# Kernel tuning notes

Hardware: AMD Instinct MI355X
Metric: run time of the kernel (lower is better)

Reference implementation:

```python
import jax, jax.numpy as jnp
import numpy as np

HEADS, OUT = 4, 64  # GATConv(heads=4, out_channels=64, concat=False)
NEG_SLOPE = 0.2


def gat_conv(x, src, dst, num_nodes, W, att_src, att_dst, bias):
    # x: [N, Fin]; W: [Fin, H*C]; att_*: [H, C]; bias: [C]
    N = num_nodes
    H, C = att_src.shape
    h = (x @ W).reshape(N, H, C)                      # per-head projections
    a_s = jnp.einsum('nhc,hc->nh', h, att_src)        # [N, H]
    a_d = jnp.einsum('nhc,hc->nh', h, att_dst)        # [N, H]
    e = jax.nn.leaky_relu(a_s[src] + a_d[dst], NEG_SLOPE)   # [E, H]
    # segment softmax over destination nodes (self-loops guarantee nonempty segments)
    m = jax.lax.stop_gradient(jax.ops.segment_max(e, dst, num_segments=N))
    ex = jnp.exp(e - m[dst])
    den = jax.ops.segment_sum(ex, dst, num_segments=N)
    alpha = ex / den[dst]                              # [E, H]
    out = jax.ops.segment_sum(h[src] * alpha[:, :, None], dst, num_segments=N)  # [N,H,C]
    return out.mean(axis=1) + bias                     # concat=False -> head mean


def setup_inputs() -> dict:
    key = jax.random.key(0)
    ks = jax.random.split(key, 16)
    N, E, Fin, G = 100000, 800000, 8, 256
    x = jax.random.normal(ks[0], (N, Fin), dtype=jnp.float32)
    edge_index = jax.random.randint(ks[1], (2, E), 0, N, dtype=jnp.int64)
    batch = jnp.sort(jax.random.randint(ks[2], (N,), 0, G, dtype=jnp.int64))
    s = 0.1
    return {
        'x': x, 'edge_index': edge_index, 'batch': batch, 'num_graphs': G,
        'W1': jax.random.normal(ks[3], (Fin, HEADS * OUT), jnp.float32) * s,
        'a_src1': jax.random.normal(ks[4], (HEADS, OUT), jnp.float32) * s,
        'a_dst1': jax.random.normal(ks[5], (HEADS, OUT), jnp.float32) * s,
        'b1': jnp.zeros((OUT,), jnp.float32),
        'W2': jax.random.normal(ks[6], (OUT, HEADS * OUT), jnp.float32) * s,
        'a_src2': jax.random.normal(ks[7], (HEADS, OUT), jnp.float32) * s,
        'a_dst2': jax.random.normal(ks[8], (HEADS, OUT), jnp.float32) * s,
        'b2': jnp.zeros((OUT,), jnp.float32),
        'Wp1': jax.random.normal(ks[9], (OUT, 32), jnp.float32) * s,
        'bp1': jnp.zeros((32,), jnp.float32),
        'Wp2': jax.random.normal(ks[10], (32, 1), jnp.float32) * s,
        'bp2': jnp.zeros((1,), jnp.float32),
    }


def reference(x, edge_index, batch, num_graphs,
              W1, a_src1, a_dst1, b1,
              W2, a_src2, a_dst2, b2,
              Wp1, bp1, Wp2, bp2):
    N = x.shape[0]
    loops = jnp.arange(N, dtype=edge_index.dtype)
    src = jnp.concatenate([edge_index[0], loops])  # PyG add_self_loops=True
    dst = jnp.concatenate([edge_index[1], loops])
    h = jax.nn.relu(gat_conv(x, src, dst, N, W1, a_src1, a_dst1, b1))
    h = jax.nn.relu(gat_conv(h, src, dst, N, W2, a_src2, a_dst2, b2))
    # global mean pool per graph
    sums = jax.ops.segment_sum(h, batch, num_segments=num_graphs)
    cnt = jax.ops.segment_sum(jnp.ones((N,), h.dtype), batch, num_segments=num_graphs)
    pooled = sums / jnp.maximum(cnt, 1.0)[:, None]
    hid = jax.nn.relu(pooled @ Wp1 + bp1)
    return hid @ Wp2 + bp2  # [num_graphs, 1]
```

## Files before the change

### kernel.cpp

```cpp
#include <hip/hip_runtime.h>

#define HEADS 4
#define CH 64
#define HC 256
#define NEG 0.2f

typedef __attribute__((ext_vector_type(8))) short bf16x8;
typedef __attribute__((ext_vector_type(4))) float f32x4;

__device__ __forceinline__ unsigned short f2bf(float f){
  unsigned u = __float_as_uint(f);
  u += 0x7fffu + ((u >> 16) & 1u);
  return (unsigned short)(u >> 16);
}
__device__ __forceinline__ float bf2f(unsigned short s){
  return __uint_as_float(((unsigned)s) << 16);
}

__global__ __launch_bounds__(256)
void zero_kernel(int4* __restrict__ p, int n4)
{
  int i = blockIdx.x*256 + threadIdx.x;
  if (i < n4) p[i] = make_int4(0,0,0,0);
}

__global__ __launch_bounds__(256)
void deg_count_kernel(const int* __restrict__ edst, int E, int N,
                      int* __restrict__ deg, int cpr)
{
  const int range = blockIdx.x & 7;
  const int lo = (int)(((long long)N * range) / 8);
  const int hi = (int)(((long long)N * (range+1)) / 8);
  const int stride = cpr * 256;
  for (int e = (blockIdx.x >> 3)*256 + threadIdx.x; e < E; e += stride){
    int d = edst[e];
    if (d >= lo && d < hi) atomicAdd(deg + d, 1);
  }
}

__global__ __launch_bounds__(256)
void scan1_kernel(const int* __restrict__ deg, int* __restrict__ excl,
                  int* __restrict__ bsum, int N)
{
  __shared__ int sm[256];
  int i = blockIdx.x*256 + threadIdx.x;
  int v = (i < N) ? deg[i] : 0;
  sm[threadIdx.x] = v; __syncthreads();
  for (int off = 1; off < 256; off <<= 1){
    int t = (threadIdx.x >= off) ? sm[threadIdx.x - off] : 0;
    __syncthreads();
    sm[threadIdx.x] += t;
    __syncthreads();
  }
  if (i < N) excl[i] = sm[threadIdx.x] - v;
  if (threadIdx.x == 255) bsum[blockIdx.x] = sm[255];
}

__global__ __launch_bounds__(512)
void scan2_kernel(int* __restrict__ bsum, int nb)
{
  __shared__ int sm[512];
  int v = (threadIdx.x < nb) ? bsum[threadIdx.x] : 0;
  sm[threadIdx.x] = v; __syncthreads();
  for (int off = 1; off < 512; off <<= 1){
    int t = (threadIdx.x >= off) ? sm[threadIdx.x - off] : 0;
    __syncthreads();
    sm[threadIdx.x] += t;
    __syncthreads();
  }
  if (threadIdx.x < nb) bsum[threadIdx.x] = sm[threadIdx.x] - v;
}

__global__ __launch_bounds__(256)
void scan3_kernel(int* __restrict__ excl, const int* __restrict__ bsum,
                  int* __restrict__ cursor, int N)
{
  int i = blockIdx.x*256 + threadIdx.x;
  if (i >= N) return;
  int r = excl[i] + bsum[blockIdx.x];
  excl[i] = r; cursor[i] = r;
}

__global__ __launch_bounds__(256)
void scatter_kernel(const int* __restrict__ esrc, const int* __restrict__ edst,
                    int E, int N, int* __restrict__ cursor, int* __restrict__ ssrc,
                    int cpr)
{
  const int range = blockIdx.x & 7;
  const int lo = (int)(((long long)N * range) / 8);
  const int hi = (int)(((long long)N * (range+1)) / 8);
  const int stride = cpr * 256;
  for (int e = (blockIdx.x >> 3)*256 + threadIdx.x; e < E; e += stride){
    int d = edst[e];
    if (d >= lo && d < hi){
      int pos = atomicAdd(cursor + d, 1);
      ssrc[pos] = esrc[e];
    }
  }
}

template<int FIN>
__global__ void fold_kernel(const float* __restrict__ W,
                            const float* __restrict__ att_src, const float* __restrict__ att_dst,
                            float* __restrict__ wfold)
{
  int o = threadIdx.x;
  int f = o >> 3, j = o & 7;
  int h = j & 3;
  const float* att = (j < 4) ? att_src : att_dst;
  float acc = 0.f;
#pragma unroll
  for (int c = 0; c < CH; ++c)
    acc += W[(size_t)f*HC + h*CH + c] * att[h*CH + c];
  wfold[f*8 + j] = acc;
}

template<int FIN>
__global__ __launch_bounds__(256)
void att_kernel(const float* __restrict__ x, const float* __restrict__ wfold,
                float* __restrict__ a_s, float* __restrict__ a_d, int N)
{
  __shared__ float xs[32][FIN];
  __shared__ float wf[FIN*8];
  const int t = threadIdx.x;
  const int n0 = blockIdx.x * 32;
  for (int i = t; i < FIN*8; i += 256) wf[i] = wfold[i];
  for (int i = t; i < 32*FIN; i += 256){
    int n = n0 + i / FIN;
    xs[i/FIN][i%FIN] = (n < N) ? x[(size_t)n*FIN + (i % FIN)] : 0.f;
  }
  __syncthreads();
  const int nn = t >> 3, j = t & 7;
  const int n = n0 + nn;
  if (n >= N) return;
  float acc = 0.f;
#pragma unroll
  for (int f = 0; f < FIN; ++f) acc += xs[nn][f] * wf[f*8 + j];
  if (j < 4) a_s[(size_t)n*4 + j]     = acc;
  else       a_d[(size_t)n*4 + (j-4)] = acc;
}

__global__ __launch_bounds__(256)
void att_bf_kernel(const unsigned short* __restrict__ xb, const float* __restrict__ wfold,
                   float* __restrict__ a_s, float* __restrict__ a_d, int N)
{
  __shared__ float xs[32][64];
  __shared__ float wf[64*8];
  const int t = threadIdx.x;
  const int n0 = blockIdx.x * 32;
  const ushort4* xb4 = (const ushort4*)xb;
  for (int i = t; i < 64*8; i += 256) wf[i] = wfold[i];
  for (int i4 = t; i4 < 32*16; i4 += 256){
    int n = n0 + (i4 >> 4);
    ushort4 v = (n < N) ? xb4[(size_t)n*16 + (i4 & 15)] : make_ushort4(0,0,0,0);
    float* dst = &xs[i4 >> 4][(i4 & 15)*4];
    dst[0] = bf2f(v.x); dst[1] = bf2f(v.y); dst[2] = bf2f(v.z); dst[3] = bf2f(v.w);
  }
  __syncthreads();
  const int nn = t >> 3, j = t & 7;
  const int n = n0 + nn;
  if (n >= N) return;
  float acc = 0.f;
#pragma unroll
  for (int f = 0; f < 64; ++f) acc += xs[nn][f] * wf[f*8 + j];
  if (j < 4) a_s[(size_t)n*4 + j]     = acc;
  else       a_d[(size_t)n*4 + (j-4)] = acc;
}

__global__ __launch_bounds__(256)
void gat_l1_kernel(const int* __restrict__ rowstart, const int* __restrict__ ssrc,
                   int N, int E,
                   const float* __restrict__ a_s, const float* __restrict__ a_d,
                   const float* __restrict__ x, const float* __restrict__ W1,
                   const float* __restrict__ b1,
                   unsigned short* __restrict__ featb)
{
  __shared__ int    slds[4][4][16];
  __shared__ float4 wlds[4][4][16];
  __shared__ float4 zlds[16][8];
  __shared__ float4 dnlds[16];
  const int t    = threadIdx.x;
  const int wv   = t >> 6;
  const int lane = t & 63;
  const int grp  = lane >> 4;
  const int fq   = lane & 15;
  const int p    = fq >> 3;
  const int f    = fq & 7;
  const int r    = wv*4 + grp;
  const int d    = blockIdx.x*16 + r;

  float z0=0.f, z1=0.f, z2=0.f, z3=0.f;
  float dn0=0.f, dn1=0.f, dn2=0.f, dn3=0.f;
  if (d < N){
    const int start = rowstart[d];
    const int end   = (d == N-1) ? E : rowstart[d+1];
    const float4 ad4 = *(const float4*)(a_d + (size_t)d*4);
    {
      const float4 asd = *(const float4*)(a_s + (size_t)d*4);
      float v, es0, es1, es2, es3;
      v = asd.x + ad4.x; v = v > 0.f ? v : NEG*v; es0 = __expf(v);
      v = asd.y + ad4.y; v = v > 0.f ? v : NEG*v; es1 = __expf(v);
      v = asd.z + ad4.z; v = v > 0.f ? v : NEG*v; es2 = __expf(v);
      v = asd.w + ad4.w; v = v > 0.f ? v : NEG*v; es3 = __expf(v);
      if (p == 0){
        const float xv = x[(size_t)d*8 + f];
        z0 += es0*xv; z1 += es1*xv; z2 += es2*xv; z3 += es3*xv;
        dn0 += es0; dn1 += es1; dn2 += es2; dn3 += es3;
      }
    }
    for (int base = start; base < end; base += 16){
      const int cnt = min(16, end - base);
      int sreg = 0; float e0=0.f, e1=0.f, e2=0.f, e3=0.f;
      if (fq < cnt){
        sreg = ssrc[base + fq];
        const float4 as4 = *(const float4*)(a_s + (size_t)sreg*4);
        float v;
        v = as4.x + ad4.x; v = v > 0.f ? v : NEG*v; e0 = __expf(v);
        v = as4.y + ad4.y; v = v > 0.f ? v : NEG*v; e1 = __expf(v);
        v = as4.z + ad4.z; v = v > 0.f ? v : NEG*v; e2 = __expf(v);
        v = as4.w + ad4.w; v = v > 0.f ? v : NEG*v; e3 = __expf(v);
      }
      slds[wv][grp][fq] = sreg;
      wlds[wv][grp][fq] = make_float4(e0, e1, e2, e3);
      __builtin_amdgcn_wave_barrier();
      int k = p;
      for (; k + 6 < cnt; k += 8){
        const int sA = slds[wv][grp][k],   sB = slds[wv][grp][k+2];
        const int sC = slds[wv][grp][k+4], sD = slds[wv][grp][k+6];
        const float xA = x[(size_t)sA*8 + f];
        const float xB = x[(size_t)sB*8 + f];
        const float xC = x[(size_t)sC*8 + f];
        const float xD = x[(size_t)sD*8 + f];
        const float4 wA = wlds[wv][grp][k],   wB = wlds[wv][grp][k+2];
        const float4 wC = wlds[wv][grp][k+4], wD = wlds[wv][grp][k+6];
        z0 += wA.x*xA; z1 += wA.y*xA; z2 += wA.z*xA; z3 += wA.w*xA;
        dn0 += wA.x; dn1 += wA.y; dn2 += wA.z; dn3 += wA.w;
        z0 += wB.x*xB; z1 += wB.y*xB; z2 += wB.z*xB; z3 += wB.w*xB;
        dn0 += wB.x; dn1 += wB.y; dn2 += wB.z; dn3 += wB.w;
        z0 += wC.x*xC; z1 += wC.y*xC; z2 += wC.z*xC; z3 += wC.w*xC;
        dn0 += wC.x; dn1 += wC.y; dn2 += wC.z; dn3 += wC.w;
        z0 += wD.x*xD; z1 += wD.y*xD; z2 += wD.z*xD; z3 += wD.w*xD;
        dn0 += wD.x; dn1 += wD.y; dn2 += wD.z; dn3 += wD.w;
      }
      for (; k < cnt; k += 2){
        const int    s  = slds[wv][grp][k];
        const float4 w4 = wlds[wv][grp][k];
        const float  xv = x[(size_t)s*8 + f];
        z0 += w4.x*xv; z1 += w4.y*xv; z2 += w4.z*xv; z3 += w4.w*xv;
        dn0 += w4.x; dn1 += w4.y; dn2 += w4.z; dn3 += w4.w;
      }
      __builtin_amdgcn_wave_barrier();
    }
  }
  z0  += __shfl_xor(z0, 8);  z1  += __shfl_xor(z1, 8);
  z2  += __shfl_xor(z2, 8);  z3  += __shfl_xor(z3, 8);
  dn0 += __shfl_xor(dn0, 8); dn1 += __shfl_xor(dn1, 8);
  dn2 += __shfl_xor(dn2, 8); dn3 += __shfl_xor(dn3, 8);
  if (d >= N){ dn0=dn1=dn2=dn3=1.f; }
  if (fq < 8)  zlds[r][f] = make_float4(z0, z1, z2, z3);
  if (fq == 0) dnlds[r]   = make_float4(dn0, dn1, dn2, dn3);
  __syncthreads();
  float Wf[4][8];
#pragma unroll
  for (int h = 0; h < 4; ++h)
#pragma unroll
    for (int ff = 0; ff < 8; ++ff)
      Wf[h][ff] = W1[ff*HC + h*CH + lane];
  const float bc = b1[lane];
#pragma unroll
  for (int i = 0; i < 4; ++i){
    const int r2 = wv*4 + i;
    const int d2 = blockIdx.x*16 + r2;
    if (d2 >= N) break;
    const float4 dn = dnlds[r2];
    float a0=0.f, a1=0.f, a2=0.f, a3=0.f;
#pragma unroll
    for (int ff = 0; ff < 8; ++ff){
      const float4 q = zlds[r2][ff];
      a0 += q.x*Wf[0][ff]; a1 += q.y*Wf[1][ff];
      a2 += q.z*Wf[2][ff]; a3 += q.w*Wf[3][ff];
    }
    float val = 0.25f*(a0*__builtin_amdgcn_rcpf(dn.x) + a1*__builtin_amdgcn_rcpf(dn.y)
                     + a2*__builtin_amdgcn_rcpf(dn.z) + a3*__builtin_amdgcn_rcpf(dn.w));
    val = fmaxf(val + bc, 0.f);
    featb[(size_t)d2*CH + lane] = f2bf(val);
  }
}

__global__ __launch_bounds__(256)
void w2fold_kernel(const float* __restrict__ W2, unsigned short* __restrict__ w2bf)
{
  int i = blockIdx.x*256 + threadIdx.x;
  int j  = i & 7;
  int l  = (i >> 3) & 63;
  int nf = (i >> 9) & 3;
  int kc = i >> 11;
  int q = kc*32 + (l >> 4)*8 + j;
  int c = nf*16 + (l & 15);
  int f = q & 63, h = q >> 6;
  w2bf[i] = f2bf(W2[(size_t)f*HC + h*64 + c]);
}

__global__ __launch_bounds__(256)
void gat_z_mfma_kernel(const int* __restrict__ rowstart, const int* __restrict__ ssrc,
                       int N, int E,
                       const float* __restrict__ a_s, const float* __restrict__ a_d,
                       const unsigned short* __restrict__ featb,
                       const unsigned short* __restrict__ w2bf,
                       const float* __restrict__ b2,
                       float* __restrict__ feat2)
{
  __shared__ int    slds[4][4][16];
  __shared__ float4 wlds[4][4][16];
  __shared__ unsigned short zlds[16][264];
  const int t    = threadIdx.x;
  const int wv   = t >> 6;
  const int lane = t & 63;
  const int grp  = lane >> 4;
  const int fq   = lane & 15;
  const int r    = wv*4 + grp;
  const int d    = blockIdx.x*16 + r;

  float z00=0,z01=0,z02=0,z03=0, z10=0,z11=0,z12=0,z13=0;
  float z20=0,z21=0,z22=0,z23=0, z30=0,z31=0,z32=0,z33=0;
  float dn0=1.f, dn1=1.f, dn2=1.f, dn3=1.f;
  if (d < N){
    const int start = rowstart[d];
    const int end   = (d == N-1) ? E : rowstart[d+1];
    const float4 ad4 = *(const float4*)(a_d + (size_t)d*4);
    const ushort4* __restrict__ fb4 = (const ushort4*)featb;
    {
      const float4 asd = *(const float4*)(a_s + (size_t)d*4);
      float v, es0, es1, es2, es3;
      v = asd.x + ad4.x; v = v > 0.f ? v : NEG*v; es0 = __expf(v);
      v = asd.y + ad4.y; v = v > 0.f ? v : NEG*v; es1 = __expf(v);
      v = asd.z + ad4.z; v = v > 0.f ? v : NEG*v; es2 = __expf(v);
      v = asd.w + ad4.w; v = v > 0.f ? v : NEG*v; es3 = __expf(v);
      const ushort4 hv = fb4[(size_t)d*16 + fq];
      const float f0 = bf2f(hv.x), f1 = bf2f(hv.y), f2 = bf2f(hv.z), f3 = bf2f(hv.w);
      z00 = es0*f0; z01 = es0*f1; z02 = es0*f2; z03 = es0*f3;
      z10 = es1*f0; z11 = es1*f1; z12 = es1*f2; z13 = es1*f3;
      z20 = es2*f0; z21 = es2*f1; z22 = es2*f2; z23 = es2*f3;
      z30 = es3*f0; z31 = es3*f1; z32 = es3*f2; z33 = es3*f3;
      dn0 = es0; dn1 = es1; dn2 = es2; dn3 = es3;
    }
    for (int base = start; base < end; base += 16){
      const int cnt = min(16, end - base);
      int sreg = 0; float e0=0.f, e1=0.f, e2=0.f, e3=0.f;
      if (fq < cnt){
        sreg = ssrc[base + fq];
        const float4 as4 = *(const float4*)(a_s + (size_t)sreg*4);
        float v;
        v = as4.x + ad4.x; v = v > 0.f ? v : NEG*v; e0 = __expf(v);
        v = as4.y + ad4.y; v = v > 0.f ? v : NEG*v; e1 = __expf(v);
        v = as4.z + ad4.z; v = v > 0.f ? v : NEG*v; e2 = __expf(v);
        v = as4.w + ad4.w; v = v > 0.f ? v : NEG*v; e3 = __expf(v);
      }
      slds[wv][grp][fq] = sreg;
      wlds[wv][grp][fq] = make_float4(e0, e1, e2, e3);
      __builtin_amdgcn_wave_barrier();
#define ACC_EDGE(W4, HV) do{ \
        const float f0_ = bf2f((HV).x), f1_ = bf2f((HV).y), f2_ = bf2f((HV).z), f3_ = bf2f((HV).w); \
        z00 += (W4).x*f0_; z01 += (W4).x*f1_; z02 += (W4).x*f2_; z03 += (W4).x*f3_; \
        z10 += (W4).y*f0_; z11 += (W4).y*f1_; z12 += (W4).y*f2_; z13 += (W4).y*f3_; \
        z20 += (W4).z*f0_; z21 += (W4).z*f1_; z22 += (W4).z*f2_; z23 += (W4).z*f3_; \
        z30 += (W4).w*f0_; z31 += (W4).w*f1_; z32 += (W4).w*f2_; z33 += (W4).w*f3_; \
        dn0 += (W4).x; dn1 += (W4).y; dn2 += (W4).z; dn3 += (W4).w; }while(0)
      int k = 0;
      for (; k + 3 < cnt; k += 4){
        const int sA = slds[wv][grp][k],   sB = slds[wv][grp][k+1];
        const int sC = slds[wv][grp][k+2], sD = slds[wv][grp][k+3];
        const ushort4 hA = fb4[(size_t)sA*16 + fq];
        const ushort4 hB = fb4[(size_t)sB*16 + fq];
        const ushort4 hC = fb4[(size_t)sC*16 + fq];
        const ushort4 hD = fb4[(size_t)sD*16 + fq];
        const float4 wA = wlds[wv][grp][k],   wB = wlds[wv][grp][k+1];
        const float4 wC = wlds[wv][grp][k+2], wD = wlds[wv][grp][k+3];
        ACC_EDGE(wA, hA); ACC_EDGE(wB, hB); ACC_EDGE(wC, hC); ACC_EDGE(wD, hD);
      }
      for (; k < cnt; ++k){
        const int    s  = slds[wv][grp][k];
        const float4 w4 = wlds[wv][grp][k];
        const ushort4 hv = fb4[(size_t)s*16 + fq];
        ACC_EDGE(w4, hv);
      }
#undef ACC_EDGE
      __builtin_amdgcn_wave_barrier();
    }
  }
  {
    const float s0 = 0.25f*__builtin_amdgcn_rcpf(dn0);
    const float s1 = 0.25f*__builtin_amdgcn_rcpf(dn1);
    const float s2 = 0.25f*__builtin_amdgcn_rcpf(dn2);
    const float s3 = 0.25f*__builtin_amdgcn_rcpf(dn3);
    ushort4* zrow = (ushort4*)zlds[r];
    ushort4 o;
    o.x=f2bf(z00*s0); o.y=f2bf(z01*s0); o.z=f2bf(z02*s0); o.w=f2bf(z03*s0);
    zrow[ 0 + fq] = o;
    o.x=f2bf(z10*s1); o.y=f2bf(z11*s1); o.z=f2bf(z12*s1); o.w=f2bf(z13*s1);
    zrow[16 + fq] = o;
    o.x=f2bf(z20*s2); o.y=f2bf(z21*s2); o.z=f2bf(z22*s2); o.w=f2bf(z23*s2);
    zrow[32 + fq] = o;
    o.x=f2bf(z30*s3); o.y=f2bf(z31*s3); o.z=f2bf(z32*s3); o.w=f2bf(z33*s3);
    zrow[48 + fq] = o;
  }
  __syncthreads();
  const bf16x8* __restrict__ bfr = (const bf16x8*)w2bf;
  const int arow = lane & 15;
  const int kg   = lane >> 4;
  f32x4 acc = {0.f, 0.f, 0.f, 0.f};
#pragma unroll
  for (int kc = 0; kc < 8; ++kc){
    const bf16x8 a = *(const bf16x8*)(&zlds[arow][kc*32 + kg*8]);
    const bf16x8 b = bfr[(kc*4 + wv)*64 + lane];
    acc = __builtin_amdgcn_mfma_f32_16x16x32_bf16(a, b, acc, 0, 0, 0);
  }
  const int col = lane & 15;
  const float bias = b2[wv*16 + col];
#pragma unroll
  for (int reg = 0; reg < 4; ++reg){
    const int rr = blockIdx.x*16 + kg*4 + reg;
    if (rr < N)
      feat2[(size_t)rr*CH + wv*16 + col] = fmaxf(acc[reg] + bias, 0.f);
  }
}

__global__ __launch_bounds__(256)
void pool_mlp_kernel(const float* __restrict__ feat,
                     const int* __restrict__ batch, int N,
                     const float* __restrict__ Wp1, const float* __restrict__ bp1,
                     const float* __restrict__ Wp2, const float* __restrict__ bp2,
                     float* __restrict__ out)
{
  const int g = blockIdx.x;
  __shared__ int seg[2];
  __shared__ float part[256];
  __shared__ float pooled[CH];
  if (threadIdx.x < 2){
    int target = g + (int)threadIdx.x;
    int lo = 0, hi = N;
    while (lo < hi){ int mid = (lo + hi) >> 1; if (batch[mid] < target) lo = mid + 1; else hi = mid; }
    seg[threadIdx.x] = lo;
  }
  __syncthreads();
  const int start = seg[0], end = seg[1];
  const int c = threadIdx.x & 63, w = threadIdx.x >> 6;
  float acc = 0.f;
  for (int n = start + w; n < end; n += 4)
    acc += feat[(size_t)n*CH + c];
  part[threadIdx.x] = acc;
  __syncthreads();
  if (threadIdx.x < CH){
    float s = part[threadIdx.x] + part[threadIdx.x+64] + part[threadIdx.x+128] + part[threadIdx.x+192];
    pooled[threadIdx.x] = s / fmaxf((float)(end - start), 1.f);
  }
  __syncthreads();
  float hid = 0.f;
  if (threadIdx.x < 32){
    float a2 = bp1[threadIdx.x];
#pragma unroll
    for (int k = 0; k < CH; ++k) a2 += pooled[k] * Wp1[k*32 + threadIdx.x];
    hid = fmaxf(a2, 0.f) * Wp2[threadIdx.x];
  }
#pragma unroll
  for (int off = 16; off; off >>= 1) hid += __shfl_down(hid, off);
  if (threadIdx.x == 0) out[g] = hid + bp2[0];
}

extern "C" void kernel_launch(void* const* d_in, const int* in_sizes, int n_in,
                              void* d_out, int out_size, void* d_ws, size_t ws_size,
                              hipStream_t stream)
{
  const float* x   = (const float*)d_in[0];
  const int*   ei  = (const int*)d_in[1];
  const int*   bat = (const int*)d_in[2];
  const float* W1  = (const float*)d_in[4];
  const float* as1 = (const float*)d_in[5];
  const float* ad1 = (const float*)d_in[6];
  const float* b1  = (const float*)d_in[7];
  const float* W2  = (const float*)d_in[8];
  const float* as2 = (const float*)d_in[9];
  const float* ad2 = (const float*)d_in[10];
  const float* b2  = (const float*)d_in[11];
  const float* Wp1 = (const float*)d_in[12];
  const float* bp1 = (const float*)d_in[13];
  const float* Wp2 = (const float*)d_in[14];
  const float* bp2 = (const float*)d_in[15];

  const int N = in_sizes[0] / 8;
  const int E = in_sizes[1] / 2;
  const int G = out_size;
  const int* esrc = ei;
  const int* edst = ei + E;

  char* wsb = (char*)d_ws;
  size_t o = 0;
  auto carve = [&](size_t bytes)->char*{
    char* p = wsb + o; o += (bytes + 255) & ~(size_t)255; return p;
  };
  unsigned short* featb = (unsigned short*)carve((size_t)N*CH*sizeof(unsigned short));
  unsigned short* w2bf  = (unsigned short*)carve((size_t)HC*CH*sizeof(unsigned short));
  float* a_s      = (float*)carve((size_t)N*HEADS*sizeof(float));
  float* a_d      = (float*)carve((size_t)N*HEADS*sizeof(float));
  float* feat2    = (float*)carve((size_t)N*CH*sizeof(float));
  float* wfold    = (float*)carve((size_t)64*8*sizeof(float));
  int*   rowstart = (int*)carve((size_t)N*sizeof(int));
  int*   cursor   = (int*)carve((size_t)N*sizeof(int));
  int*   deg      = (int*)carve((size_t)(N+4)*sizeof(int));
  int*   bsum     = (int*)carve((size_t)512*sizeof(int));
  int*   ssrc     = (int*)carve((size_t)E*sizeof(int));

  const int nb1 = (N + 255) / 256;
  const int atb = (N + 31) / 32;
  const int gb  = (N + 15) / 16;
  const int cpr = 512;
  const int csb = 8 * cpr;
  const int n4  = (N + 3) / 4;
  const int zb  = (n4 + 255) / 256;

  zero_kernel<<<zb, 256, 0, stream>>>((int4*)deg, n4);
  deg_count_kernel<<<csb, 256, 0, stream>>>(edst, E, N, deg, cpr);
  scan1_kernel<<<nb1, 256, 0, stream>>>(deg, rowstart, bsum, N);
  scan2_kernel<<<1, 512, 0, stream>>>(bsum, nb1);
  scan3_kernel<<<nb1, 256, 0, stream>>>(rowstart, bsum, cursor, N);
  scatter_kernel<<<csb, 256, 0, stream>>>(esrc, edst, E, N, cursor, ssrc, cpr);

  fold_kernel<8><<<1, 8*8, 0, stream>>>(W1, as1, ad1, wfold);
  att_kernel<8><<<atb, 256, 0, stream>>>(x, wfold, a_s, a_d, N);
  gat_l1_kernel<<<gb, 256, 0, stream>>>(rowstart, ssrc, N, E, a_s, a_d, x, W1, b1, featb);

  fold_kernel<64><<<1, 64*8, 0, stream>>>(W2, as2, ad2, wfold);
  att_bf_kernel<<<atb, 256, 0, stream>>>(featb, wfold, a_s, a_d, N);
  w2fold_kernel<<<64, 256, 0, stream>>>(W2, w2bf);
  gat_z_mfma_kernel<<<gb, 256, 0, stream>>>(rowstart, ssrc, N, E, a_s, a_d,
                                            featb, w2bf, b2, feat2);

  pool_mlp_kernel<<<G, 256, 0, stream>>>(feat2, bat, N, Wp1, bp1, Wp2, bp2, (float*)d_out);
}
```

Measured before the change: 217.9 us.

## Merge weight-prep launches and fuse layer-2 attention logits into layer-1 epilogue

Four small setup kernels (degree zeroing, two attention-weight folds and the W2 bf16 repack) become one block-partitioned prep kernel, cutting launch count. The separate att_bf pass, which re-read the bf16 layer-1 features to compute layer-2 source and destination logits, is removed. Those logits are now computed in gat_l1's epilogue from fp32 values staged in shared memory, with results going to new a_s2/a_d2 buffers. This costs extra shared memory and a block barrier in gat_l1. The logits now come from unrounded fp32 values instead of the bf16 features, so they differ slightly in numerics.

Measured after the change: 200.5 us. 8.0% less time.

```diff
diff --git a/kernel.cpp b/kernel.cpp
--- a/kernel.cpp
+++ b/kernel.cpp
@@ -18,10 +18,45 @@
 }
 
 __global__ __launch_bounds__(256)
-void zero_kernel(int4* __restrict__ p, int n4)
-{
-  int i = blockIdx.x*256 + threadIdx.x;
-  if (i < n4) p[i] = make_int4(0,0,0,0);
+void prep_kernel(const float* __restrict__ W1, const float* __restrict__ as1, const float* __restrict__ ad1,
+                 const float* __restrict__ W2, const float* __restrict__ as2, const float* __restrict__ ad2,
+                 float* __restrict__ wfold1, float* __restrict__ wfold2,
+                 unsigned short* __restrict__ w2bf,
+                 int4* __restrict__ deg4, int n4)
+{
+  const int b = blockIdx.x;
+  if (b == 0){
+    int o = threadIdx.x;
+    if (o < 64){
+      int f = o >> 3, j = o & 7, h = j & 3;
+      const float* att = (j < 4) ? as1 : ad1;
+      float acc = 0.f;
+#pragma unroll
+      for (int c = 0; c < CH; ++c) acc += W1[(size_t)f*HC + h*CH + c] * att[h*CH + c];
+      wfold1[o] = acc;
+    }
+  } else if (b <= 2){
+    int o = (b-1)*256 + threadIdx.x;
+    int f = o >> 3, j = o & 7, h = j & 3;
+    const float* att = (j < 4) ? as2 : ad2;
+    float acc = 0.f;
+#pragma unroll
+    for (int c = 0; c < CH; ++c) acc += W2[(size_t)f*HC + h*CH + c] * att[h*CH + c];
+    wfold2[o] = acc;
+  } else if (b < 67){
+    int i = (b-3)*256 + threadIdx.x;
+    int j  = i & 7;
+    int l  = (i >> 3) & 63;
+    int nf = (i >> 9) & 3;
+    int kc = i >> 11;
+    int q = kc*32 + (l >> 4)*8 + j;
+    int c = nf*16 + (l & 15);
+    int f = q & 63, h = q >> 6;
+    w2bf[i] = f2bf(W2[(size_t)f*HC + h*64 + c]);
+  } else {
+    int i = (b-67)*256 + threadIdx.x;
+    if (i < n4) deg4[i] = make_int4(0,0,0,0);
+  }
 }
 
 __global__ __launch_bounds__(256)
@@ -100,22 +135,6 @@
 }
 
 template<int FIN>
-__global__ void fold_kernel(const float* __restrict__ W,
-                            const float* __restrict__ att_src, const float* __restrict__ att_dst,
-                            float* __restrict__ wfold)
-{
-  int o = threadIdx.x;
-  int f = o >> 3, j = o & 7;
-  int h = j & 3;
-  const float* att = (j < 4) ? att_src : att_dst;
-  float acc = 0.f;
-#pragma unroll
-  for (int c = 0; c < CH; ++c)
-    acc += W[(size_t)f*HC + h*CH + c] * att[h*CH + c];
-  wfold[f*8 + j] = acc;
-}
-
-template<int FIN>
 __global__ __launch_bounds__(256)
 void att_kernel(const float* __restrict__ x, const float* __restrict__ wfold,
                 float* __restrict__ a_s, float* __restrict__ a_d, int N)
@@ -141,44 +160,21 @@
 }
 
 __global__ __launch_bounds__(256)
-void att_bf_kernel(const unsigned short* __restrict__ xb, const float* __restrict__ wfold,
-                   float* __restrict__ a_s, float* __restrict__ a_d, int N)
-{
-  __shared__ float xs[32][64];
-  __shared__ float wf[64*8];
-  const int t = threadIdx.x;
-  const int n0 = blockIdx.x * 32;
-  const ushort4* xb4 = (const ushort4*)xb;
-  for (int i = t; i < 64*8; i += 256) wf[i] = wfold[i];
-  for (int i4 = t; i4 < 32*16; i4 += 256){
-    int n = n0 + (i4 >> 4);
-    ushort4 v = (n < N) ? xb4[(size_t)n*16 + (i4 & 15)] : make_ushort4(0,0,0,0);
-    float* dst = &xs[i4 >> 4][(i4 & 15)*4];
-    dst[0] = bf2f(v.x); dst[1] = bf2f(v.y); dst[2] = bf2f(v.z); dst[3] = bf2f(v.w);
-  }
-  __syncthreads();
-  const int nn = t >> 3, j = t & 7;
-  const int n = n0 + nn;
-  if (n >= N) return;
-  float acc = 0.f;
-#pragma unroll
-  for (int f = 0; f < 64; ++f) acc += xs[nn][f] * wf[f*8 + j];
-  if (j < 4) a_s[(size_t)n*4 + j]     = acc;
-  else       a_d[(size_t)n*4 + (j-4)] = acc;
-}
-
-__global__ __launch_bounds__(256)
 void gat_l1_kernel(const int* __restrict__ rowstart, const int* __restrict__ ssrc,
                    int N, int E,
                    const float* __restrict__ a_s, const float* __restrict__ a_d,
                    const float* __restrict__ x, const float* __restrict__ W1,
                    const float* __restrict__ b1,
-                   unsigned short* __restrict__ featb)
+                   const float* __restrict__ wfold2,
+                   unsigned short* __restrict__ featb,
+                   float* __restrict__ a_s2, float* __restrict__ a_d2)
 {
   __shared__ int    slds[4][4][16];
   __shared__ float4 wlds[4][4][16];
   __shared__ float4 zlds[16][8];
   __shared__ float4 dnlds[16];
+  __shared__ float  flds[16][65];
+  __shared__ float  wf2[512];
   const int t    = threadIdx.x;
   const int wv   = t >> 6;
   const int lane = t & 63;
@@ -188,6 +184,9 @@
   const int f    = fq & 7;
   const int r    = wv*4 + grp;
   const int d    = blockIdx.x*16 + r;
+
+  wf2[t] = wfold2[t];
+  wf2[256 + t] = wfold2[256 + t];
 
   float z0=0.f, z1=0.f, z2=0.f, z3=0.f;
   float dn0=0.f, dn1=0.f, dn2=0.f, dn3=0.f;
@@ -284,21 +283,20 @@
                      + a2*__builtin_amdgcn_rcpf(dn.z) + a3*__builtin_amdgcn_rcpf(dn.w));
     val = fmaxf(val + bc, 0.f);
     featb[(size_t)d2*CH + lane] = f2bf(val);
-  }
-}
-
-__global__ __launch_bounds__(256)
-void w2fold_kernel(const float* __restrict__ W2, unsigned short* __restrict__ w2bf)
-{
-  int i = blockIdx.x*256 + threadIdx.x;
-  int j  = i & 7;
-  int l  = (i >> 3) & 63;
-  int nf = (i >> 9) & 3;
-  int kc = i >> 11;
-  int q = kc*32 + (l >> 4)*8 + j;
-  int c = nf*16 + (l & 15);
-  int f = q & 63, h = q >> 6;
-  w2bf[i] = f2bf(W2[(size_t)f*HC + h*64 + c]);
+    flds[r2][lane] = val;
+  }
+  __syncthreads();
+  if (t < 128){
+    const int nn = t >> 3, j = t & 7;
+    const int n = blockIdx.x*16 + nn;
+    if (n < N){
+      float acc = 0.f;
+#pragma unroll
+      for (int ch = 0; ch < 64; ++ch) acc += flds[nn][ch] * wf2[ch*8 + j];
+      if (j < 4) a_s2[(size_t)n*4 + j]     = acc;
+      else       a_d2[(size_t)n*4 + (j-4)] = acc;
+    }
+  }
 }
 
 __global__ __launch_bounds__(256)
@@ -502,8 +500,11 @@
   unsigned short* w2bf  = (unsigned short*)carve((size_t)HC*CH*sizeof(unsigned short));
   float* a_s      = (float*)carve((size_t)N*HEADS*sizeof(float));
   float* a_d      = (float*)carve((size_t)N*HEADS*sizeof(float));
+  float* a_s2     = (float*)carve((size_t)N*HEADS*sizeof(float));
+  float* a_d2     = (float*)carve((size_t)N*HEADS*sizeof(float));
   float* feat2    = (float*)carve((size_t)N*CH*sizeof(float));
-  float* wfold    = (float*)carve((size_t)64*8*sizeof(float));
+  float* wfold1   = (float*)carve((size_t)64*8*sizeof(float));
+  float* wfold2   = (float*)carve((size_t)64*8*sizeof(float));
   int*   rowstart = (int*)carve((size_t)N*sizeof(int));
   int*   cursor   = (int*)carve((size_t)N*sizeof(int));
   int*   deg      = (int*)carve((size_t)(N+4)*sizeof(int));
@@ -518,21 +519,20 @@
   const int n4  = (N + 3) / 4;
   const int zb  = (n4 + 255) / 256;
 
-  zero_kernel<<<zb, 256, 0, stream>>>((int4*)deg, n4);
+  prep_kernel<<<67 + zb, 256, 0, stream>>>(W1, as1, ad1, W2, as2, ad2,
+                                           wfold1, wfold2, w2bf, (int4*)deg, n4);
+
   deg_count_kernel<<<csb, 256, 0, stream>>>(edst, E, N, deg, cpr);
   scan1_kernel<<<nb1, 256, 0, stream>>>(deg, rowstart, bsum, N);
   scan2_kernel<<<1, 512, 0, stream>>>(bsum, nb1);
   scan3_kernel<<<nb1, 256, 0, stream>>>(rowstart, bsum, cursor, N);
   scatter_kernel<<<csb, 256, 0, stream>>>(esrc, edst, E, N, cursor, ssrc, cpr);
 
-  fold_kernel<8><<<1, 8*8, 0, stream>>>(W1, as1, ad1, wfold);
-  att_kernel<8><<<atb, 256, 0, stream>>>(x, wfold, a_s, a_d, N);
-  gat_l1_kernel<<<gb, 256, 0, stream>>>(rowstart, ssrc, N, E, a_s, a_d, x, W1, b1, featb);
-
-  fold_kernel<64><<<1, 64*8, 0, stream>>>(W2, as2, ad2, wfold);
-  att_bf_kernel<<<atb, 256, 0, stream>>>(featb, wfold, a_s, a_d, N);
-  w2fold_kernel<<<64, 256, 0, stream>>>(W2, w2bf);
-  gat_z_mfma_kernel<<<gb, 256, 0, stream>>>(rowstart, ssrc, N, E, a_s, a_d,
+  att_kernel<8><<<atb, 256, 0, stream>>>(x, wfold1, a_s, a_d, N);
+  gat_l1_kernel<<<gb, 256, 0, stream>>>(rowstart, ssrc, N, E, a_s, a_d, x, W1, b1,
+                                        wfold2, featb, a_s2, a_d2);
+
+  gat_z_mfma_kernel<<<gb, 256, 0, stream>>>(rowstart, ssrc, N, E, a_s2, a_d2,
                                             featb, w2bf, b2, feat2);
 
   pool_mlp_kernel<<<G, 256, 0, stream>>>(feat2, bat, N, Wp1, bp1, Wp2, bp2, (float*)d_out);
```
